# Optimization experiments

Hardware: AMD Instinct MI355X
Metric: run time of the kernel (lower is better)

## Reference

```python
import jax, jax.numpy as jnp
import numpy as np

EPS = 1e-7

def segment_softmax(logits, seg, num_segments):
    # Numerically-stable softmax over edges grouped by destination node,
    # applied independently per feature column (logits: [E, D]).
    m = jax.ops.segment_max(logits, seg, num_segments=num_segments)  # [N, D]
    e = jnp.exp(logits - m[seg])                                     # [E, D]
    s = jax.ops.segment_sum(e, seg, num_segments=num_segments)       # [N, D]
    return e / s[seg]

def setup_inputs() -> dict:
    key = jax.random.key(0)
    N, E, D_IN, D_OUT = 50000, 800000, 64, 64
    ks = jax.random.split(key, 4)
    x = jax.random.normal(ks[0], (N, D_IN), dtype=jnp.float32)
    edge_index = jax.random.randint(ks[1], (2, E), 0, N, dtype=jnp.int64)
    # nn.Linear(in_feat, out_feat) params
    W = jax.random.normal(ks[2], (D_OUT, D_IN), dtype=jnp.float32) * (1.0 / np.sqrt(D_IN))
    b = jax.random.normal(ks[3], (D_OUT,), dtype=jnp.float32) * 0.01
    beta = jnp.ones((1,), dtype=jnp.float32)  # aggr='softmax_sg' beta parameter
    return {"x": x, "W": W, "b": b, "beta": beta, "edge_index": edge_index}

def reference(x, W, b, beta, edge_index):
    N = x.shape[0]
    dst = edge_index[0]  # scatter / softmax segment ids
    src = edge_index[1]  # gather ids
    # gather + ReLU + eps
    edge_msg = jax.nn.relu(x[src]) + EPS                    # [E, D]
    # softmax_sg aggregation: softmax of beta*msg over incoming edges of each dst
    a = segment_softmax(beta * edge_msg, dst, N)            # [E, D]
    h = jax.ops.segment_sum(edge_msg * a, dst, num_segments=N)  # [N, D]
    # final Linear
    return h @ W.T + b
```

## Files before the change

kernel.cpp:

```cpp
#include <hip/hip_runtime.h>
#include <hip/hip_fp16.h>

#define EPS 1e-7f
#define EPB 4096
#define CSTRIDE 16

__device__ __forceinline__ void pack_body(const float4* __restrict__ x4,
                                          short4* __restrict__ xh, int i, int nq) {
    if (i < nq) {
        float4 v = x4[i];
        short4 o;
        o.x = __half_as_short(__float2half_rn(fmaxf(v.x, 0.f) + EPS));
        o.y = __half_as_short(__float2half_rn(fmaxf(v.y, 0.f) + EPS));
        o.z = __half_as_short(__float2half_rn(fmaxf(v.z, 0.f) + EPS));
        o.w = __half_as_short(__float2half_rn(fmaxf(v.w, 0.f) + EPS));
        xh[i] = o;
    }
}

__global__ __launch_bounds__(256) void part_kernel(const float4* __restrict__ x4,
                                                   short4* __restrict__ xh, int nq,
                                                   int packBlocks,
                                                   const int* __restrict__ ei, int E,
                                                   int CAPB,
                                                   int* __restrict__ cursor,
                                                   unsigned int* __restrict__ partArr) {
    int bb = blockIdx.x;
    int tid = threadIdx.x;
    if (bb < packBlocks) {
        pack_body(x4, xh, bb * 256 + tid, nq);
        return;
    }
    __shared__ int hist[256];
    __shared__ int off[256];
    int blk = bb - packBlocks;
    hist[tid] = 0;
    __syncthreads();

    int base = blk * EPB;
    int dd[16], ss[16], bk[16], rk[16];
    #pragma unroll
    for (int k = 0; k < 16; ++k) {
        int e = base + k * 256 + tid;
        bk[k] = -1;
        if (e < E) {
            dd[k] = ei[e];
            ss[k] = ei[E + e];
            bk[k] = dd[k] >> 8;
            rk[k] = atomicAdd(&hist[bk[k]], 1);
        }
    }
    __syncthreads();
    int hv = hist[tid];
    if (hv > 0) off[tid] = atomicAdd(&cursor[tid * CSTRIDE], hv);
    __syncthreads();
    #pragma unroll
    for (int k = 0; k < 16; ++k) {
        if (bk[k] >= 0) {
            int idx = off[bk[k]] + rk[k];
            if (idx < CAPB)
                partArr[(size_t)bk[k] * CAPB + idx] =
                    ((unsigned int)dd[k] << 16) | (unsigned int)ss[k];
        }
    }
}

__global__ __launch_bounds__(256) void build_kernel(const unsigned int* __restrict__ partArr,
                                                    const int* __restrict__ cursor,
                                                    int CAPB,
                                                    unsigned short* __restrict__ slots,
                                                    int* __restrict__ deg) {
    __shared__ int c[256];
    int tid = threadIdx.x;
    int bkt = blockIdx.x;
    c[tid] = 0;
    __syncthreads();
    int cnt = cursor[bkt * CSTRIDE];
    if (cnt > CAPB) cnt = CAPB;
    const unsigned int* pa = partArr + (size_t)bkt * CAPB;
    for (int i = tid; i < cnt; i += 256) {
        unsigned int u = pa[i];
        int d = u >> 16;
        int r = atomicAdd(&c[d & 255], 1);
        if (r < 64) slots[((size_t)d << 6) + r] = (unsigned short)(u & 0xFFFF);
    }
    __syncthreads();
    int dv = c[tid];
    if (dv > 64) dv = 64;
    deg[(bkt << 8) + tid] = dv;
}

__global__ __launch_bounds__(256) void main_kernel(const __half* __restrict__ xh,
                                                   const float* __restrict__ beta_p,
                                                   const int* __restrict__ deg,
                                                   const unsigned short* __restrict__ slots,
                                                   float* __restrict__ out, int N) {
    int tid  = threadIdx.x;
    int lane = tid & 63;
    int n = blockIdx.x * 4 + (tid >> 6);
    if (n >= N) return;
    float beta = beta_p[0];

    unsigned short raw = slots[((size_t)n << 6) + lane];
    int dg = deg[n];
    int myid = (lane < dg) ? (int)raw : 0;

    float s = 0.0f, t = 0.0f;
    #define ACCV(w, j) { float m = __half2float(w); float e = __expf(beta * m); \
                         e = (i + (j) < dg) ? e : 0.0f;   \
                         s += e; t = fmaf(m, e, t); }
    for (int i = 0; i < dg; i += 8) {
        const __half* q0 = xh + (__builtin_amdgcn_readlane(myid, i + 0) << 6);
        const __half* q1 = xh + (__builtin_amdgcn_readlane(myid, i + 1) << 6);
        const __half* q2 = xh + (__builtin_amdgcn_readlane(myid, i + 2) << 6);
        const __half* q3 = xh + (__builtin_amdgcn_readlane(myid, i + 3) << 6);
        const __half* q4 = xh + (__builtin_amdgcn_readlane(myid, i + 4) << 6);
        const __half* q5 = xh + (__builtin_amdgcn_readlane(myid, i + 5) << 6);
        const __half* q6 = xh + (__builtin_amdgcn_readlane(myid, i + 6) << 6);
        const __half* q7 = xh + (__builtin_amdgcn_readlane(myid, i + 7) << 6);
        __half w0 = q0[lane], w1 = q1[lane], w2 = q2[lane], w3 = q3[lane];
        __half w4 = q4[lane], w5 = q5[lane], w6 = q6[lane], w7 = q7[lane];
        ACCV(w0, 0) ACCV(w1, 1) ACCV(w2, 2) ACCV(w3, 3)
        ACCV(w4, 4) ACCV(w5, 5) ACCV(w6, 6) ACCV(w7, 7)
    }
    #undef ACCV
    float h = (dg > 0) ? (t / s) : 0.0f;
    out[(size_t)n * 64 + lane] = h;
}

#define GS 65
__global__ __launch_bounds__(256) void gemm_kernel(float* __restrict__ out,
                                                   const float* __restrict__ W,
                                                   const float* __restrict__ b,
                                                   int N) {
    __shared__ float hl[64 * GS];
    __shared__ float Wt[64 * GS];
    int tid  = threadIdx.x;
    int row0 = blockIdx.x * 64;

    #pragma unroll
    for (int kk = 0; kk < 4; ++kk) {
        int i4 = kk * 256 + tid;
        int rj = i4 >> 4;
        int d0 = (i4 & 15) * 4;
        float4 wv = *(const float4*)(W + (size_t)i4 * 4);
        Wt[(d0 + 0) * GS + rj] = wv.x;
        Wt[(d0 + 1) * GS + rj] = wv.y;
        Wt[(d0 + 2) * GS + rj] = wv.z;
        Wt[(d0 + 3) * GS + rj] = wv.w;
        float4 hv = (row0 + rj < N)
                  ? *(const float4*)(out + (size_t)row0 * 64 + (size_t)i4 * 4)
                  : make_float4(0.f, 0.f, 0.f, 0.f);
        hl[rj * GS + d0 + 0] = hv.x;
        hl[rj * GS + d0 + 1] = hv.y;
        hl[rj * GS + d0 + 2] = hv.z;
        hl[rj * GS + d0 + 3] = hv.w;
    }
    __syncthreads();

    int c4 = tid & 15;
    int r4 = tid >> 4;
    float4 bv = *(const float4*)(b + c4 * 4);
    float acc[4][4];
    #pragma unroll
    for (int ri = 0; ri < 4; ++ri) {
        acc[ri][0] = bv.x; acc[ri][1] = bv.y; acc[ri][2] = bv.z; acc[ri][3] = bv.w;
    }
    #pragma unroll 8
    for (int d = 0; d < 64; ++d) {
        float h0 = hl[(r4 * 4 + 0) * GS + d];
        float h1 = hl[(r4 * 4 + 1) * GS + d];
        float h2 = hl[(r4 * 4 + 2) * GS + d];
        float h3 = hl[(r4 * 4 + 3) * GS + d];
        float w0 = Wt[d * GS + c4 * 4 + 0];
        float w1 = Wt[d * GS + c4 * 4 + 1];
        float w2 = Wt[d * GS + c4 * 4 + 2];
        float w3 = Wt[d * GS + c4 * 4 + 3];
        acc[0][0] = fmaf(h0, w0, acc[0][0]); acc[0][1] = fmaf(h0, w1, acc[0][1]);
        acc[0][2] = fmaf(h0, w2, acc[0][2]); acc[0][3] = fmaf(h0, w3, acc[0][3]);
        acc[1][0] = fmaf(h1, w0, acc[1][0]); acc[1][1] = fmaf(h1, w1, acc[1][1]);
        acc[1][2] = fmaf(h1, w2, acc[1][2]); acc[1][3] = fmaf(h1, w3, acc[1][3]);
        acc[2][0] = fmaf(h2, w0, acc[2][0]); acc[2][1] = fmaf(h2, w1, acc[2][1]);
        acc[2][2] = fmaf(h2, w2, acc[2][2]); acc[2][3] = fmaf(h2, w3, acc[2][3]);
        acc[3][0] = fmaf(h3, w0, acc[3][0]); acc[3][1] = fmaf(h3, w1, acc[3][1]);
        acc[3][2] = fmaf(h3, w2, acc[3][2]); acc[3][3] = fmaf(h3, w3, acc[3][3]);
    }
    #pragma unroll
    for (int ri = 0; ri < 4; ++ri) {
        int row = row0 + r4 * 4 + ri;
        if (row < N) {
            *(float4*)(out + (size_t)row * 64 + c4 * 4) =
                make_float4(acc[ri][0], acc[ri][1], acc[ri][2], acc[ri][3]);
        }
    }
}

extern "C" void kernel_launch(void* const* d_in, const int* in_sizes, int n_in,
                              void* d_out, int out_size, void* d_ws, size_t ws_size,
                              hipStream_t stream) {
    const float* x      = (const float*)d_in[0];
    const float* W      = (const float*)d_in[1];
    const float* b      = (const float*)d_in[2];
    const float* beta_p = (const float*)d_in[3];
    const int*   ei     = (const int*)d_in[4];

    int NT = in_sizes[0];
    int N  = NT / 64;
    int E  = in_sizes[4] / 2;

    int NB = (N + 255) >> 8;
    int pblocks = (NT / 4 + 255) / 256;
    int eblocks = (E + EPB - 1) / EPB;
    int NP = NB << 8;

    size_t curB   = (size_t)256 * CSTRIDE * 4;
    size_t fixedB = curB + (size_t)NP * 4 + (size_t)NT * 2 + (size_t)NP * 64 * 2;
    int CAPB = (int)(((size_t)2 * E / NB + 4095) & ~(size_t)4095);
    if (ws_size < fixedB + (size_t)NB * CAPB * 4) {
        size_t avail = (ws_size > fixedB) ? (ws_size - fixedB) : 0;
        int fitc = (int)(avail / ((size_t)NB * 4));
        CAPB = (fitc / 64) * 64;
        if (CAPB <= 0) return;
    }

    char* p = (char*)d_ws;
    int* cursor           = (int*)p;                      p += curB;
    int* deg              = (int*)p;                      p += (size_t)NP * 4;
    unsigned int* partArr = (unsigned int*)p;             p += (size_t)NB * CAPB * 4;
    __half* xh            = (__half*)p;                   p += (size_t)NT * 2;
    unsigned short* slots = (unsigned short*)p;

    hipMemsetAsync(cursor, 0, curB, stream);

    part_kernel<<<pblocks + eblocks, 256, 0, stream>>>(
        (const float4*)x, (short4*)xh, NT / 4, pblocks, ei, E, CAPB, cursor, partArr);

    build_kernel<<<NB, 256, 0, stream>>>(partArr, cursor, CAPB, slots, deg);

    main_kernel<<<(N + 3) / 4, 256, 0, stream>>>(xh, beta_p, deg, slots,
                                                 (float*)d_out, N);

    gemm_kernel<<<(N + 63) / 64, 256, 0, stream>>>((float*)d_out, W, b, N);
}
```

Baseline: 138.2 us.

## Fuse final linear into aggregation kernel and split build across sub-blocks

The separate GEMM kernel is removed. Each wavefront now stages W transposed in shared memory and computes the 64x64 projection of its node's aggregated row using readlane broadcasts, which avoids a round trip of h through global memory and one launch. The build kernel is split four ways per bucket, using a two-pass count then atomic base reservation on deg, and deg is zeroed in the memset. The cost is that every main block reloads all of W into LDS, plus extra global atomics, and slot order within a node becomes nondeterministic.

```diff
diff --git a/kernel.cpp b/kernel.cpp
--- a/kernel.cpp
+++ b/kernel.cpp
@@ -4,6 +4,7 @@
 #define EPS 1e-7f
 #define EPB 4096
 #define CSTRIDE 16
+#define SUBB 4
 
 __device__ __forceinline__ void pack_body(const float4* __restrict__ x4,
                                           short4* __restrict__ xh, int i, int nq) {
@@ -60,7 +61,7 @@
             int idx = off[bk[k]] + rk[k];
             if (idx < CAPB)
                 partArr[(size_t)bk[k] * CAPB + idx] =
-                    ((unsigned int)dd[k] << 16) | (unsigned int)ss[k];
+                    ((unsigned int)dd[k] << 16) | (unsigned int)(ss[k] & 0xFFFF);
         }
     }
 }
@@ -71,44 +72,72 @@
                                                     unsigned short* __restrict__ slots,
                                                     int* __restrict__ deg) {
     __shared__ int c[256];
+    __shared__ int base[256];
     int tid = threadIdx.x;
-    int bkt = blockIdx.x;
+    int bkt = blockIdx.x >> 2;
+    int sub = blockIdx.x & (SUBB - 1);
     c[tid] = 0;
     __syncthreads();
+
     int cnt = cursor[bkt * CSTRIDE];
     if (cnt > CAPB) cnt = CAPB;
+    int lo = (cnt * sub) >> 2;
+    int hi = (cnt * (sub + 1)) >> 2;
     const unsigned int* pa = partArr + (size_t)bkt * CAPB;
-    for (int i = tid; i < cnt; i += 256) {
+
+    for (int i = lo + tid; i < hi; i += 256)
+        atomicAdd(&c[(pa[i] >> 16) & 255], 1);
+    __syncthreads();
+    int cc = c[tid];
+    base[tid] = (cc > 0) ? atomicAdd(&deg[(bkt << 8) + tid], cc) : 0;
+    c[tid] = 0;
+    __syncthreads();
+    for (int i = lo + tid; i < hi; i += 256) {
         unsigned int u = pa[i];
         int d = u >> 16;
-        int r = atomicAdd(&c[d & 255], 1);
+        int r = base[d & 255] + atomicAdd(&c[d & 255], 1);
         if (r < 64) slots[((size_t)d << 6) + r] = (unsigned short)(u & 0xFFFF);
     }
-    __syncthreads();
-    int dv = c[tid];
-    if (dv > 64) dv = 64;
-    deg[(bkt << 8) + tid] = dv;
 }
 
 __global__ __launch_bounds__(256) void main_kernel(const __half* __restrict__ xh,
                                                    const float* __restrict__ beta_p,
                                                    const int* __restrict__ deg,
                                                    const unsigned short* __restrict__ slots,
+                                                   const float* __restrict__ W,
+                                                   const float* __restrict__ bias,
                                                    float* __restrict__ out, int N) {
+    __shared__ float Wl[4096];
     int tid  = threadIdx.x;
     int lane = tid & 63;
-    int n = blockIdx.x * 4 + (tid >> 6);
+    int w = tid >> 6;
+    int n = blockIdx.x * 4 + w;
+    int nc = (n < N) ? n : (N - 1);
+
+    unsigned short raw = slots[((size_t)nc << 6) + lane];
+    int dg = deg[nc];
+
+    #pragma unroll
+    for (int kk = 0; kk < 4; ++kk) {
+        int ti = kk * 256 + tid;
+        float4 wv = ((const float4*)W)[ti];
+        int j = ti >> 4, f0 = (ti & 15) << 2;
+        Wl[(f0 + 0) * 64 + j] = wv.x;
+        Wl[(f0 + 1) * 64 + j] = wv.y;
+        Wl[(f0 + 2) * 64 + j] = wv.z;
+        Wl[(f0 + 3) * 64 + j] = wv.w;
+    }
+    __syncthreads();
     if (n >= N) return;
+
     float beta = beta_p[0];
-
-    unsigned short raw = slots[((size_t)n << 6) + lane];
-    int dg = deg[n];
+    if (dg > 64) dg = 64;
     int myid = (lane < dg) ? (int)raw : 0;
 
     float s = 0.0f, t = 0.0f;
-    #define ACCV(w, j) { float m = __half2float(w); float e = __expf(beta * m); \
-                         e = (i + (j) < dg) ? e : 0.0f;   \
-                         s += e; t = fmaf(m, e, t); }
+    #define ACCV(wv, j) { float m = __half2float(wv); float e = __expf(beta * m); \
+                          e = (i + (j) < dg) ? e : 0.0f;   \
+                          s += e; t = fmaf(m, e, t); }
     for (int i = 0; i < dg; i += 8) {
         const __half* q0 = xh + (__builtin_amdgcn_readlane(myid, i + 0) << 6);
         const __half* q1 = xh + (__builtin_amdgcn_readlane(myid, i + 1) << 6);
@@ -125,74 +154,14 @@
     }
     #undef ACCV
     float h = (dg > 0) ? (t / s) : 0.0f;
-    out[(size_t)n * 64 + lane] = h;
-}
-
-#define GS 65
-__global__ __launch_bounds__(256) void gemm_kernel(float* __restrict__ out,
-                                                   const float* __restrict__ W,
-                                                   const float* __restrict__ b,
-                                                   int N) {
-    __shared__ float hl[64 * GS];
-    __shared__ float Wt[64 * GS];
-    int tid  = threadIdx.x;
-    int row0 = blockIdx.x * 64;
-
-    #pragma unroll
-    for (int kk = 0; kk < 4; ++kk) {
-        int i4 = kk * 256 + tid;
-        int rj = i4 >> 4;
-        int d0 = (i4 & 15) * 4;
-        float4 wv = *(const float4*)(W + (size_t)i4 * 4);
-        Wt[(d0 + 0) * GS + rj] = wv.x;
-        Wt[(d0 + 1) * GS + rj] = wv.y;
-        Wt[(d0 + 2) * GS + rj] = wv.z;
-        Wt[(d0 + 3) * GS + rj] = wv.w;
-        float4 hv = (row0 + rj < N)
-                  ? *(const float4*)(out + (size_t)row0 * 64 + (size_t)i4 * 4)
-                  : make_float4(0.f, 0.f, 0.f, 0.f);
-        hl[rj * GS + d0 + 0] = hv.x;
-        hl[rj * GS + d0 + 1] = hv.y;
-        hl[rj * GS + d0 + 2] = hv.z;
-        hl[rj * GS + d0 + 3] = hv.w;
-    }
-    __syncthreads();
-
-    int c4 = tid & 15;
-    int r4 = tid >> 4;
-    float4 bv = *(const float4*)(b + c4 * 4);
-    float acc[4][4];
-    #pragma unroll
-    for (int ri = 0; ri < 4; ++ri) {
-        acc[ri][0] = bv.x; acc[ri][1] = bv.y; acc[ri][2] = bv.z; acc[ri][3] = bv.w;
-    }
-    #pragma unroll 8
-    for (int d = 0; d < 64; ++d) {
-        float h0 = hl[(r4 * 4 + 0) * GS + d];
-        float h1 = hl[(r4 * 4 + 1) * GS + d];
-        float h2 = hl[(r4 * 4 + 2) * GS + d];
-        float h3 = hl[(r4 * 4 + 3) * GS + d];
-        float w0 = Wt[d * GS + c4 * 4 + 0];
-        float w1 = Wt[d * GS + c4 * 4 + 1];
-        float w2 = Wt[d * GS + c4 * 4 + 2];
-        float w3 = Wt[d * GS + c4 * 4 + 3];
-        acc[0][0] = fmaf(h0, w0, acc[0][0]); acc[0][1] = fmaf(h0, w1, acc[0][1]);
-        acc[0][2] = fmaf(h0, w2, acc[0][2]); acc[0][3] = fmaf(h0, w3, acc[0][3]);
-        acc[1][0] = fmaf(h1, w0, acc[1][0]); acc[1][1] = fmaf(h1, w1, acc[1][1]);
-        acc[1][2] = fmaf(h1, w2, acc[1][2]); acc[1][3] = fmaf(h1, w3, acc[1][3]);
-        acc[2][0] = fmaf(h2, w0, acc[2][0]); acc[2][1] = fmaf(h2, w1, acc[2][1]);
-        acc[2][2] = fmaf(h2, w2, acc[2][2]); acc[2][3] = fmaf(h2, w3, acc[2][3]);
-        acc[3][0] = fmaf(h3, w0, acc[3][0]); acc[3][1] = fmaf(h3, w1, acc[3][1]);
-        acc[3][2] = fmaf(h3, w2, acc[3][2]); acc[3][3] = fmaf(h3, w3, acc[3][3]);
-    }
-    #pragma unroll
-    for (int ri = 0; ri < 4; ++ri) {
-        int row = row0 + r4 * 4 + ri;
-        if (row < N) {
-            *(float4*)(out + (size_t)row * 64 + c4 * 4) =
-                make_float4(acc[ri][0], acc[ri][1], acc[ri][2], acc[ri][3]);
-        }
-    }
+
+    float o = bias[lane];
+    int hb = __float_as_int(h);
+    #pragma unroll 16
+    for (int f = 0; f < 64; ++f)
+        o = fmaf(__int_as_float(__builtin_amdgcn_readlane(hb, f)),
+                 Wl[(f << 6) + lane], o);
+    out[(size_t)n * 64 + lane] = o;
 }
 
 extern "C" void kernel_launch(void* const* d_in, const int* in_sizes, int n_in,
@@ -208,37 +177,35 @@
     int N  = NT / 64;
     int E  = in_sizes[4] / 2;
 
-    int NB = (N + 255) >> 8;
+    int NBK = (N + 255) >> 8;
+    int NP  = NBK << 8;
     int pblocks = (NT / 4 + 255) / 256;
     int eblocks = (E + EPB - 1) / EPB;
-    int NP = NB << 8;
-
-    size_t curB   = (size_t)256 * CSTRIDE * 4;
+
+    size_t curB   = (size_t)NBK * CSTRIDE * 4;
     size_t fixedB = curB + (size_t)NP * 4 + (size_t)NT * 2 + (size_t)NP * 64 * 2;
-    int CAPB = (int)(((size_t)2 * E / NB + 4095) & ~(size_t)4095);
-    if (ws_size < fixedB + (size_t)NB * CAPB * 4) {
+    int CAPB = (int)(((size_t)2 * E / NBK + 255) & ~(size_t)255);
+    if (ws_size < fixedB + (size_t)NBK * CAPB * 4) {
         size_t avail = (ws_size > fixedB) ? (ws_size - fixedB) : 0;
-        int fitc = (int)(avail / ((size_t)NB * 4));
+        int fitc = (int)(avail / ((size_t)NBK * 4));
         CAPB = (fitc / 64) * 64;
         if (CAPB <= 0) return;
     }
 
     char* p = (char*)d_ws;
-    int* cursor           = (int*)p;                      p += curB;
-    int* deg              = (int*)p;                      p += (size_t)NP * 4;
-    unsigned int* partArr = (unsigned int*)p;             p += (size_t)NB * CAPB * 4;
-    __half* xh            = (__half*)p;                   p += (size_t)NT * 2;
+    int* cursor           = (int*)p;              p += curB;
+    int* deg              = (int*)p;              p += (size_t)NP * 4;
+    unsigned int* partArr = (unsigned int*)p;     p += (size_t)NBK * CAPB * 4;
+    __half* xh            = (__half*)p;           p += (size_t)NT * 2;
     unsigned short* slots = (unsigned short*)p;
 
-    hipMemsetAsync(cursor, 0, curB, stream);
+    hipMemsetAsync(cursor, 0, curB + (size_t)NP * 4, stream);
 
     part_kernel<<<pblocks + eblocks, 256, 0, stream>>>(
         (const float4*)x, (short4*)xh, NT / 4, pblocks, ei, E, CAPB, cursor, partArr);
 
-    build_kernel<<<NB, 256, 0, stream>>>(partArr, cursor, CAPB, slots, deg);
-
-    main_kernel<<<(N + 3) / 4, 256, 0, stream>>>(xh, beta_p, deg, slots,
+    build_kernel<<<NBK * SUBB, 256, 0, stream>>>(partArr, cursor, CAPB, slots, deg);
+
+    main_kernel<<<(N + 3) / 4, 256, 0, stream>>>(xh, beta_p, deg, slots, W, b,
                                                  (float*)d_out, N);
-
-    gemm_kernel<<<(N + 63) / 64, 256, 0, stream>>>((float*)d_out, W, b, N);
-}
+}
```

Measured after the change: 156.5 us. 1.13x slower.
